# Optimization experiments

Hardware: AMD Instinct MI355X
Metric: run time of the kernel (lower is better)

## Reference

```python
import jax, jax.numpy as jnp
import numpy as np

B, T, N, D, L, TE, F, H = 32, 1024, 256, 512, 512, 512, 2048, 8

PARAM_SHAPES = {
    "sa_norm_g": (D,), "sa_norm_b": (D,),
    "sa_q_w": (D, D), "sa_q_b": (D,), "sa_k_w": (D, D), "sa_k_b": (D,), "sa_v_w": (D, D), "sa_v_b": (D,),
    "sa_emb_w": (TE, 2 * D), "sa_emb_b": (2 * D,), "sa_pnorm_g": (D,), "sa_pnorm_b": (D,),
    "sa_out_w": (D, D), "sa_out_b": (D,),
    "ca_norm_g": (D,), "ca_norm_b": (D,), "ca_tnorm_g": (L,), "ca_tnorm_b": (L,),
    "ca_q_w": (D, D), "ca_q_b": (D,), "ca_k_w": (L, D), "ca_k_b": (D,), "ca_v_w": (L, D), "ca_v_b": (D,),
    "ca_emb_w": (TE, 2 * D), "ca_emb_b": (2 * D,), "ca_pnorm_g": (D,), "ca_pnorm_b": (D,),
    "ca_out_w": (D, D), "ca_out_b": (D,),
    "ffn_w1": (D, F), "ffn_b1": (F,), "ffn_w2": (F, D), "ffn_b2": (D,),
    "ffn_emb_w": (TE, 2 * D), "ffn_emb_b": (2 * D,), "ffn_pnorm_g": (D,), "ffn_pnorm_b": (D,),
    "ffn_out_w": (D, D), "ffn_out_b": (D,),
}


def setup_inputs() -> dict:
    key = jax.random.key(0)
    inp = {}
    inp["x"] = jax.random.normal(jax.random.fold_in(key, 100), (B, T, D), jnp.float32)
    inp["xf"] = jax.random.normal(jax.random.fold_in(key, 101), (B, N, L), jnp.float32)
    inp["emb"] = jax.random.normal(jax.random.fold_in(key, 102), (B, TE), jnp.float32)
    inp["src_mask"] = (jax.random.uniform(jax.random.fold_in(key, 103), (B, T, 1)) < 0.9).astype(jnp.float32)
    for i, (name, shp) in enumerate(PARAM_SHAPES.items()):
        k = jax.random.fold_in(key, i)
        if name.endswith("norm_g") or name.endswith("pnorm_g") or name.endswith("tnorm_g"):
            inp[name] = jnp.ones(shp, jnp.float32)
        else:
            inp[name] = 0.02 * jax.random.normal(k, shp, jnp.float32)
    return inp


def _ln(v, g, b):
    mu = jnp.mean(v, -1, keepdims=True)
    var = jnp.mean(jnp.square(v - mu), -1, keepdims=True)
    return (v - mu) * jax.lax.rsqrt(var + 1e-5) * g + b


def _styl(h, emb, ew, eb, ng, nb, ow, ob):
    # StylizationBlock: AdaLN scale-shift then SiLU + linear (dropout = identity at eval)
    e = (jax.nn.silu(emb) @ ew + eb)[:, None, :]          # [B, 1, 2D]
    scale, shift = jnp.split(e, 2, axis=-1)
    hn = _ln(h, ng, nb) * (1.0 + scale) + shift
    return jax.nn.silu(hn) @ ow + ob


def _lin_attn(q, k, v):
    # Performer-style: contract over sequence first -> [B,H,d,dl], then apply queries
    att = jnp.einsum('bnhd,bnhl->bhdl', k, v)
    return jnp.einsum('bthd,bhdl->bthl', q, att)


def _forward(x, xf, emb, src_mask, sa_norm_g, sa_norm_b, sa_q_w, sa_q_b, sa_k_w, sa_k_b, sa_v_w, sa_v_b, sa_emb_w, sa_emb_b, sa_pnorm_g, sa_pnorm_b, sa_out_w, sa_out_b, ca_norm_g, ca_norm_b, ca_tnorm_g, ca_tnorm_b, ca_q_w, ca_q_b, ca_k_w, ca_k_b, ca_v_w, ca_v_b, ca_emb_w, ca_emb_b, ca_pnorm_g, ca_pnorm_b, ca_out_w, ca_out_b, ffn_w1, ffn_b1, ffn_w2, ffn_b2, ffn_emb_w, ffn_emb_b, ffn_pnorm_g, ffn_pnorm_b, ffn_out_w, ffn_out_b):
    B_, T_, D_ = x.shape
    d = D_ // H
    # ---- linear temporal self-attention ----
    xn = _ln(x, sa_norm_g, sa_norm_b)
    q = jax.nn.softmax((xn @ sa_q_w + sa_q_b).reshape(B_, T_, H, d), axis=-1)   # softmax over feature dim
    k = jax.nn.softmax((xn @ sa_k_w + sa_k_b + (1.0 - src_mask) * -1000000.0).reshape(B_, T_, H, d), axis=1)  # softmax over seq
    v = ((xn @ sa_v_w + sa_v_b) * src_mask).reshape(B_, T_, H, d)
    y = _lin_attn(q, k, v).reshape(B_, T_, D_)
    x = x + _styl(y, emb, sa_emb_w, sa_emb_b, sa_pnorm_g, sa_pnorm_b, sa_out_w, sa_out_b)
    # ---- linear temporal cross-attention ----
    xn = _ln(x, ca_norm_g, ca_norm_b)
    tn = _ln(xf, ca_tnorm_g, ca_tnorm_b)
    N_ = xf.shape[1]
    q = jax.nn.softmax((xn @ ca_q_w + ca_q_b).reshape(B_, T_, H, d), axis=-1)
    k = jax.nn.softmax((tn @ ca_k_w + ca_k_b).reshape(B_, N_, H, d), axis=1)
    v = (tn @ ca_v_w + ca_v_b).reshape(B_, N_, H, d)
    y = _lin_attn(q, k, v).reshape(B_, T_, D_)
    x = x + _styl(y, emb, ca_emb_w, ca_emb_b, ca_pnorm_g, ca_pnorm_b, ca_out_w, ca_out_b)
    # ---- FFN ----
    y = jax.nn.gelu(x @ ffn_w1 + ffn_b1, approximate=False) @ ffn_w2 + ffn_b2
    x = x + _styl(y, emb, ffn_emb_w, ffn_emb_b, ffn_pnorm_g, ffn_pnorm_b, ffn_out_w, ffn_out_b)
    return x


def reference(x, xf, emb, src_mask, sa_norm_g, sa_norm_b, sa_q_w, sa_q_b, sa_k_w, sa_k_b, sa_v_w, sa_v_b, sa_emb_w, sa_emb_b, sa_pnorm_g, sa_pnorm_b, sa_out_w, sa_out_b, ca_norm_g, ca_norm_b, ca_tnorm_g, ca_tnorm_b, ca_q_w, ca_q_b, ca_k_w, ca_k_b, ca_v_w, ca_v_b, ca_emb_w, ca_emb_b, ca_pnorm_g, ca_pnorm_b, ca_out_w, ca_out_b, ffn_w1, ffn_b1, ffn_w2, ffn_b2, ffn_emb_w, ffn_emb_b, ffn_pnorm_g, ffn_pnorm_b, ffn_out_w, ffn_out_b):
    return _forward(x, xf, emb, src_mask, sa_norm_g, sa_norm_b, sa_q_w, sa_q_b, sa_k_w, sa_k_b, sa_v_w, sa_v_b, sa_emb_w, sa_emb_b, sa_pnorm_g, sa_pnorm_b, sa_out_w, sa_out_b, ca_norm_g, ca_norm_b, ca_tnorm_g, ca_tnorm_b, ca_q_w, ca_q_b, ca_k_w, ca_k_b, ca_v_w, ca_v_b, ca_emb_w, ca_emb_b, ca_pnorm_g, ca_pnorm_b, ca_out_w, ca_out_b, ffn_w1, ffn_b1, ffn_w2, ffn_b2, ffn_emb_w, ffn_emb_b, ffn_pnorm_g, ffn_pnorm_b, ffn_out_w, ffn_out_b)
```

## Files before the change

kernel.cpp:

```cpp
#include <hip/hip_runtime.h>
#include <hip/hip_bf16.h>
#include <math.h>

typedef __hip_bfloat16 bf16;
typedef __hip_bfloat162 bf16x2;
using s8 = __attribute__((ext_vector_type(8))) short;
using f4 = __attribute__((ext_vector_type(4))) float;

#define DEV __device__ __forceinline__
DEV float bf2f(bf16 h){ return __bfloat162float(h); }
DEV bf16  f2bf(float f){ return __float2bfloat16(f); }
DEV float silu_f(float x){ return x / (1.0f + __expf(-x)); }
DEV float gelu_f(float x){ return 0.5f * x * (1.0f + erff(x * 0.70710678118654752f)); }

__global__ __launch_bounds__(256) void transpose_w(const float* __restrict__ in,
                                                   bf16* __restrict__ out, int K, int N){
  __shared__ float t[32][33];
  int n0 = blockIdx.x * 32, k0 = blockIdx.y * 32;
  int tx = threadIdx.x, ty = threadIdx.y;
  for (int i = ty; i < 32; i += 8) t[i][tx] = in[(size_t)(k0 + i) * N + n0 + tx];
  __syncthreads();
  for (int i = ty; i < 32; i += 8) out[(size_t)(n0 + i) * K + k0 + tx] = f2bf(t[tx][i]);
}

__global__ __launch_bounds__(256) void ln_kernel(const float* __restrict__ in, bf16* __restrict__ out,
                                                 const float* __restrict__ g, const float* __restrict__ b){
  int row = blockIdx.x, tid = threadIdx.x;
  const float* r = in + (size_t)row * 512;
  float2 v = *(const float2*)&r[tid * 2];
  float s = v.x + v.y, s2 = v.x * v.x + v.y * v.y;
  #pragma unroll
  for (int o = 1; o < 64; o <<= 1){ s += __shfl_xor(s, o); s2 += __shfl_xor(s2, o); }
  __shared__ float rs[4], rs2[4];
  int w = tid >> 6;
  if ((tid & 63) == 0){ rs[w] = s; rs2[w] = s2; }
  __syncthreads();
  s  = rs[0] + rs[1] + rs[2] + rs[3];
  s2 = rs2[0] + rs2[1] + rs2[2] + rs2[3];
  float mu = s * (1.0f / 512.0f);
  float var = fmaxf(s2 * (1.0f / 512.0f) - mu * mu, 0.0f);
  float rstd = rsqrtf(var + 1e-5f);
  int c = tid * 2;
  bf16x2 o;
  o.x = f2bf((v.x - mu) * rstd * g[c]     + b[c]);
  o.y = f2bf((v.y - mu) * rstd * g[c + 1] + b[c + 1]);
  *(bf16x2*)&out[(size_t)row * 512 + c] = o;
}

__global__ __launch_bounds__(256) void styl_ln_kernel(const bf16* __restrict__ in, const float* __restrict__ e,
                                                      const float* __restrict__ g, const float* __restrict__ b,
                                                      bf16* __restrict__ out, int T){
  int row = blockIdx.x, tid = threadIdx.x;
  int bidx = row / T;
  const bf16* r = in + (size_t)row * 512;
  bf16x2 hv = *(const bf16x2*)&r[tid * 2];
  float x0 = bf2f(hv.x), x1 = bf2f(hv.y);
  float s = x0 + x1, s2 = x0 * x0 + x1 * x1;
  #pragma unroll
  for (int o = 1; o < 64; o <<= 1){ s += __shfl_xor(s, o); s2 += __shfl_xor(s2, o); }
  __shared__ float rs[4], rs2[4];
  int w = tid >> 6;
  if ((tid & 63) == 0){ rs[w] = s; rs2[w] = s2; }
  __syncthreads();
  s  = rs[0] + rs[1] + rs[2] + rs[3];
  s2 = rs2[0] + rs2[1] + rs2[2] + rs2[3];
  float mu = s * (1.0f / 512.0f);
  float var = fmaxf(s2 * (1.0f / 512.0f) - mu * mu, 0.0f);
  float rstd = rsqrtf(var + 1e-5f);
  int c = tid * 2;
  const float* eb = e + (size_t)bidx * 1024;
  float h0 = (x0 - mu) * rstd * g[c]     + b[c];
  float h1 = (x1 - mu) * rstd * g[c + 1] + b[c + 1];
  h0 = h0 * (1.0f + eb[c])     + eb[512 + c];
  h1 = h1 * (1.0f + eb[c + 1]) + eb[512 + c + 1];
  bf16x2 o; o.x = f2bf(silu_f(h0)); o.y = f2bf(silu_f(h1));
  *(bf16x2*)&out[(size_t)row * 512 + c] = o;
}

__global__ __launch_bounds__(256) void kv_outer(const bf16* __restrict__ k, const bf16* __restrict__ v,
                                                const float* __restrict__ mask,
                                                float* __restrict__ att_part, float* __restrict__ den_part,
                                                int T, int ld, int Tc){
  int bh = blockIdx.x;
  int b = bh >> 3, h = bh & 7;
  int chunk = blockIdx.y;
  int t_begin = chunk * Tc;
  __shared__ float kexp[64][64];
  __shared__ bf16 vb[64][64];
  int tid = threadIdx.x;
  int lg = tid & 15, tg = tid >> 4;
  int d0 = tg * 4, l0 = lg * 4;
  const float* mrow = mask ? (mask + (size_t)b * T) : nullptr;
  float acc[4][4] = {};
  float sden[4] = {0.0f, 0.0f, 0.0f, 0.0f};
  for (int tcb = t_begin; tcb < t_begin + Tc; tcb += 64){
    __syncthreads();
    #pragma unroll
    for (int i = 0; i < 2; ++i){
      int rr = (tid >> 3) + i * 32;
      int cc = (tid & 7) * 8;
      size_t goff = ((size_t)(b * T + tcb + rr)) * ld + h * 64 + cc;
      s8 kv8 = *(const s8*)&k[goff];
      *(s8*)&vb[rr][cc] = *(const s8*)&v[goff];
      float mk = mrow ? mrow[tcb + rr] : 1.0f;
      float4 e0, e1;
      e0.x = mk * __expf(bf2f(((const bf16*)&kv8)[0]));
      e0.y = mk * __expf(bf2f(((const bf16*)&kv8)[1]));
      e0.z = mk * __expf(bf2f(((const bf16*)&kv8)[2]));
      e0.w = mk * __expf(bf2f(((const bf16*)&kv8)[3]));
      e1.x = mk * __expf(bf2f(((const bf16*)&kv8)[4]));
      e1.y = mk * __expf(bf2f(((const bf16*)&kv8)[5]));
      e1.z = mk * __expf(bf2f(((const bf16*)&kv8)[6]));
      e1.w = mk * __expf(bf2f(((const bf16*)&kv8)[7]));
      *(float4*)&kexp[rr][cc]     = e0;
      *(float4*)&kexp[rr][cc + 4] = e1;
    }
    __syncthreads();
    for (int tt = 0; tt < 64; ++tt){
      float4 kf = *(const float4*)&kexp[tt][d0];
      float kk[4] = {kf.x, kf.y, kf.z, kf.w};
      float vv[4];
      #pragma unroll
      for (int j = 0; j < 4; ++j) vv[j] = bf2f(vb[tt][l0 + j]);
      #pragma unroll
      for (int a = 0; a < 4; ++a){
        sden[a] += kk[a];
        #pragma unroll
        for (int c2 = 0; c2 < 4; ++c2) acc[a][c2] += kk[a] * vv[c2];
      }
    }
  }
  size_t base = ((size_t)(chunk * 256 + bh)) * 4096;
  #pragma unroll
  for (int a = 0; a < 4; ++a)
    #pragma unroll
    for (int c2 = 0; c2 < 4; ++c2) att_part[base + (size_t)(d0 + a) * 64 + l0 + c2] = acc[a][c2];
  if (lg == 0){
    size_t dbase = ((size_t)(chunk * 256 + bh)) * 64;
    #pragma unroll
    for (int a = 0; a < 4; ++a) den_part[dbase + d0 + a] = sden[a];
  }
}

__global__ __launch_bounds__(256) void kv_reduce(const float* __restrict__ att_part,
                                                 const float* __restrict__ den_part,
                                                 float* __restrict__ att, int nchunk){
  int bh = blockIdx.x, tid = threadIdx.x;
  __shared__ float dinv[64];
  if (tid < 64){
    float d = 0.0f;
    for (int c = 0; c < nchunk; ++c) d += den_part[((size_t)(c * 256 + bh)) * 64 + tid];
    dinv[tid] = 1.0f / d;
  }
  __syncthreads();
  #pragma unroll
  for (int i = 0; i < 16; ++i){
    int e = i * 256 + tid;
    float s = 0.0f;
    for (int c = 0; c < nchunk; ++c) s += att_part[((size_t)(c * 256 + bh)) * 4096 + e];
    att[(size_t)bh * 4096 + e] = s * dinv[e >> 6];
  }
}

__global__ __launch_bounds__(256) void q_att(const bf16* __restrict__ q, const float* __restrict__ att,
                                             bf16* __restrict__ y, int T, int ldq){
  int ntc = T >> 6;
  int idx = blockIdx.x;
  int tcb = idx % ntc; int h = (idx / ntc) & 7; int b = idx / (ntc * 8);
  __shared__ float ab[64][64];
  __shared__ bf16 qb[64][64];
  int tid = threadIdx.x;
  #pragma unroll
  for (int i = 0; i < 4; ++i){
    int e = i * 1024 + tid * 4;
    *(float4*)&ab[e >> 6][e & 63] = *(const float4*)&att[((size_t)(b * 8 + h)) * 4096 + e];
  }
  #pragma unroll
  for (int i = 0; i < 2; ++i){
    int rr = (tid >> 3) + i * 32;
    int cc = (tid & 7) * 8;
    s8 v = *(const s8*)&q[((size_t)(b * T + tcb * 64 + rr)) * ldq + h * 64 + cc];
    float f[8];
    #pragma unroll
    for (int j = 0; j < 8; ++j) f[j] = bf2f(((const bf16*)&v)[j]);
    float m = f[0];
    #pragma unroll
    for (int j = 1; j < 8; ++j) m = fmaxf(m, f[j]);
    m = fmaxf(m, __shfl_xor(m, 1));
    m = fmaxf(m, __shfl_xor(m, 2));
    m = fmaxf(m, __shfl_xor(m, 4));
    float s = 0.0f;
    #pragma unroll
    for (int j = 0; j < 8; ++j){ f[j] = __expf(f[j] - m); s += f[j]; }
    s += __shfl_xor(s, 1);
    s += __shfl_xor(s, 2);
    s += __shfl_xor(s, 4);
    float inv = 1.0f / s;
    s8 o;
    #pragma unroll
    for (int j = 0; j < 8; ++j) ((bf16*)&o)[j] = f2bf(f[j] * inv);
    *(s8*)&qb[rr][cc ^ ((rr & 7) << 3)] = o;
  }
  __syncthreads();
  int lg = tid & 15, tg = tid >> 4;
  int t0 = tg * 4, l0 = lg * 4;
  float acc[4][4] = {};
  for (int dd = 0; dd < 64; ++dd){
    float qv[4], av[4];
    #pragma unroll
    for (int j = 0; j < 4; ++j){
      int row = t0 + j;
      qv[j] = bf2f(qb[row][dd ^ ((row & 7) << 3)]);
      av[j] = ab[dd][l0 + j];
    }
    #pragma unroll
    for (int a = 0; a < 4; ++a)
      #pragma unroll
      for (int c2 = 0; c2 < 4; ++c2) acc[a][c2] += qv[a] * av[c2];
  }
  #pragma unroll
  for (int a = 0; a < 4; ++a)
    #pragma unroll
    for (int c2 = 0; c2 < 4; ++c2)
      y[((size_t)(b * T + tcb * 64 + t0 + a)) * 512 + h * 64 + l0 + c2] = f2bf(acc[a][c2]);
}

__global__ __launch_bounds__(256) void emb_gemm(const float* __restrict__ emb,
    const float* __restrict__ w0, const float* __restrict__ b0,
    const float* __restrict__ w1, const float* __restrict__ b1,
    const float* __restrict__ w2, const float* __restrict__ b2,
    float* __restrict__ e_all){
  int col = blockIdx.x * 256 + threadIdx.x;
  int b = blockIdx.y, which = blockIdx.z;
  const float* W  = (which == 0) ? w0 : (which == 1 ? w1 : w2);
  const float* bb = (which == 0) ? b0 : (which == 1 ? b1 : b2);
  __shared__ float s[512];
  for (int i = threadIdx.x; i < 512; i += 256){ float v = emb[b * 512 + i]; s[i] = silu_f(v); }
  __syncthreads();
  float acc = bb[col];
  for (int kk = 0; kk < 512; ++kk) acc += s[kk] * W[(size_t)kk * 1024 + col];
  e_all[((size_t)which * 32 + b) * 1024 + col] = acc;
}

template<int EPI>
__global__ __launch_bounds__(256, 2) void gemm_bt(
    const bf16* __restrict__ A, const bf16* __restrict__ BT,
    const float* __restrict__ bias, void* __restrict__ out,
    const float* __restrict__ extra, void* __restrict__ out2, int M, int N, int K){
  __shared__ __align__(16) bf16 As[2][128 * 32];
  __shared__ __align__(16) bf16 Bs[2][128 * 32];
  int tid = threadIdx.x;
  int w = tid >> 6, lane = tid & 63;
  int wr = w >> 1, wc = w & 1;
  int nwg = gridDim.x * gridDim.y;
  int lin = blockIdx.y * gridDim.x + blockIdx.x;
  int xcd = lin & 7, sidx = lin >> 3;
  int q8 = nwg >> 3, r8 = nwg & 7;
  int wg = (xcd < r8 ? xcd * (q8 + 1) : r8 * (q8 + 1) + (xcd - r8) * q8) + sidx;
  int bn = wg % gridDim.x, bm = wg / gridDim.x;

  const bf16* Ab = A  + (size_t)bm * 128 * K;
  const bf16* Bb = BT + (size_t)bn * 128 * K;

  int srow = tid >> 2;
  int scol = (tid & 3) * 8;

  auto stage = [&](int buf, int k0){
    #pragma unroll
    for (int i = 0; i < 2; ++i){
      const bf16* ga = Ab + (size_t)(srow + i * 64) * K + k0 + scol;
      const bf16* gb = Bb + (size_t)(srow + i * 64) * K + k0 + scol;
      bf16* la = &As[buf][i * 2048 + w * 512];
      bf16* lb = &Bs[buf][i * 2048 + w * 512];
      __builtin_amdgcn_global_load_lds((const __attribute__((address_space(1))) void*)ga,
                                       (__attribute__((address_space(3))) void*)la, 16, 0, 0);
      __builtin_amdgcn_global_load_lds((const __attribute__((address_space(1))) void*)gb,
                                       (__attribute__((address_space(3))) void*)lb, 16, 0, 0);
    }
  };

  f4 acc[4][4];
  #pragma unroll
  for (int m = 0; m < 4; ++m)
    #pragma unroll
    for (int n = 0; n < 4; ++n)
      #pragma unroll
      for (int j = 0; j < 4; ++j) acc[m][n][j] = 0.0f;

  int nt = K >> 5;
  int arow = lane & 15;
  int koff = (lane >> 4) * 8;

  stage(0, 0);
  __syncthreads();
  int cur = 0;
  for (int t = 0; t < nt; ++t){
    if (t + 1 < nt) stage(cur ^ 1, (t + 1) * 32);
    s8 af[4], bfv[4];
    #pragma unroll
    for (int m = 0; m < 4; ++m)
      af[m] = *(const s8*)&As[cur][(wr * 64 + m * 16 + arow) * 32 + koff];
    #pragma unroll
    for (int n = 0; n < 4; ++n)
      bfv[n] = *(const s8*)&Bs[cur][(wc * 64 + n * 16 + arow) * 32 + koff];
    #pragma unroll
    for (int m = 0; m < 4; ++m)
      #pragma unroll
      for (int n = 0; n < 4; ++n)
        acc[m][n] = __builtin_amdgcn_mfma_f32_16x16x32_bf16(af[m], bfv[n], acc[m][n], 0, 0, 0);
    __syncthreads();
    cur ^= 1;
  }

  int r0 = bm * 128 + wr * 64 + (lane >> 4) * 4;
  int c0 = bn * 128 + wc * 64 + (lane & 15);
  #pragma unroll
  for (int m = 0; m < 4; ++m){
    #pragma unroll
    for (int n = 0; n < 4; ++n){
      int col = c0 + n * 16;
      float bv = bias[col];
      #pragma unroll
      for (int j = 0; j < 4; ++j){
        int row = r0 + m * 16 + j;
        float v = acc[m][n][j] + bv;
        size_t oi = (size_t)row * N + col;
        if (EPI == 0){
          ((bf16*)out)[oi] = f2bf(v);
        } else if (EPI == 2){
          ((bf16*)out)[oi] = f2bf(gelu_f(v));
        } else if (EPI == 3){
          ((float*)out)[oi] += v;
        } else if (EPI == 4){
          ((float*)out)[oi] = extra[oi] + v;
        } else if (EPI == 5){
          float nv = ((float*)out)[oi] + v;
          ((float*)out)[oi] = nv;
          ((bf16*)out2)[oi] = f2bf(nv);
        } else {
          float sc = (col >= 1024) ? extra[row] : 1.0f;
          ((bf16*)out)[oi] = f2bf(v * sc);
        }
      }
    }
  }
}

extern "C" void kernel_launch(void* const* d_in, const int* in_sizes, int n_in,
                              void* d_out, int out_size, void* d_ws, size_t ws_size,
                              hipStream_t stream){
  const float* x    = (const float*)d_in[0];
  const float* xf   = (const float*)d_in[1];
  const float* emb  = (const float*)d_in[2];
  const float* mask = (const float*)d_in[3];
  const float* P[40];
  for (int j = 0; j < 40; ++j) P[j] = (const float*)d_in[4 + j];
  enum { SA_NG, SA_NB, SA_QW, SA_QB, SA_KW, SA_KB, SA_VW, SA_VB, SA_EW, SA_EB, SA_PG, SA_PB, SA_OW, SA_OB,
         CA_NG, CA_NB, CA_TG, CA_TB, CA_QW, CA_QB, CA_KW, CA_KB, CA_VW, CA_VB, CA_EW, CA_EB, CA_PG, CA_PB, CA_OW, CA_OB,
         F_W1, F_B1, F_W2, F_B2, F_EW, F_EB, F_PG, F_PB, F_OW, F_OB };

  char* wp = (char*)d_ws;
  auto alloc = [&](size_t bytes){ void* p = (void*)wp; wp += (bytes + 255) & ~(size_t)255; return p; };

  const size_t SQ = (size_t)512 * 512 * 2;
  bf16* WT_saqkv = (bf16*)alloc(3 * SQ);
  bf16* WT_saout = (bf16*)alloc(SQ);
  bf16* WT_caq   = (bf16*)alloc(SQ);
  bf16* WT_cakv  = (bf16*)alloc(2 * SQ);
  bf16* WT_caout = (bf16*)alloc(SQ);
  bf16* WT_f1    = (bf16*)alloc((size_t)2048 * 512 * 2);
  bf16* WT_f2    = (bf16*)alloc((size_t)512 * 2048 * 2);
  bf16* WT_fout  = (bf16*)alloc(SQ);
  float* cat_sab = (float*)alloc(1536 * 4);
  float* cat_cab = (float*)alloc(1024 * 4);
  float* e_all   = (float*)alloc((size_t)3 * 32 * 1024 * 4);

  const size_t BTD2 = (size_t)32768 * 512 * 2;
  bf16* bxn  = (bf16*)alloc(BTD2);
  bf16* bqkv = (bf16*)alloc(3 * BTD2);
  bf16* by   = (bf16*)alloc(BTD2);
  bf16* bs   = (bf16*)alloc(BTD2);
  bf16* btn  = (bf16*)alloc((size_t)8192 * 512 * 2);
  float* att_part = (float*)alloc((size_t)4 * 256 * 4096 * 4);
  float* den_part = (float*)alloc((size_t)4 * 256 * 64 * 4);
  float* batt = (float*)alloc((size_t)256 * 4096 * 4);
  bf16* bh1 = bxn;
  bf16* bq_ca  = bqkv;
  bf16* bkv_ca = bqkv + BTD2 / 2;

  dim3 tb(32, 8);
  transpose_w<<<dim3(16, 16), tb, 0, stream>>>(P[SA_QW], WT_saqkv,               512, 512);
  transpose_w<<<dim3(16, 16), tb, 0, stream>>>(P[SA_KW], WT_saqkv + 512 * 512,   512, 512);
  transpose_w<<<dim3(16, 16), tb, 0, stream>>>(P[SA_VW], WT_saqkv + 1024 * 512,  512, 512);
  transpose_w<<<dim3(16, 16), tb, 0, stream>>>(P[SA_OW], WT_saout, 512, 512);
  transpose_w<<<dim3(16, 16), tb, 0, stream>>>(P[CA_QW], WT_caq, 512, 512);
  transpose_w<<<dim3(16, 16), tb, 0, stream>>>(P[CA_KW], WT_cakv,             512, 512);
  transpose_w<<<dim3(16, 16), tb, 0, stream>>>(P[CA_VW], WT_cakv + 512 * 512, 512, 512);
  transpose_w<<<dim3(16, 16), tb, 0, stream>>>(P[CA_OW], WT_caout, 512, 512);
  transpose_w<<<dim3(64, 16), tb, 0, stream>>>(P[F_W1], WT_f1, 512, 2048);
  transpose_w<<<dim3(16, 64), tb, 0, stream>>>(P[F_W2], WT_f2, 2048, 512);
  transpose_w<<<dim3(16, 16), tb, 0, stream>>>(P[F_OW], WT_fout, 512, 512);

  hipMemcpyAsync(cat_sab,        P[SA_QB], 512 * 4, hipMemcpyDeviceToDevice, stream);
  hipMemcpyAsync(cat_sab + 512,  P[SA_KB], 512 * 4, hipMemcpyDeviceToDevice, stream);
  hipMemcpyAsync(cat_sab + 1024, P[SA_VB], 512 * 4, hipMemcpyDeviceToDevice, stream);
  hipMemcpyAsync(cat_cab,        P[CA_KB], 512 * 4, hipMemcpyDeviceToDevice, stream);
  hipMemcpyAsync(cat_cab + 512,  P[CA_VB], 512 * 4, hipMemcpyDeviceToDevice, stream);

  emb_gemm<<<dim3(4, 32, 3), 256, 0, stream>>>(emb, P[SA_EW], P[SA_EB], P[CA_EW], P[CA_EB],
                                               P[F_EW], P[F_EB], e_all);

  dim3 g512(4, 256);

  ln_kernel<<<32768, 256, 0, stream>>>(x, bxn, P[SA_NG], P[SA_NB]);
  gemm_bt<6><<<dim3(12, 256), 256, 0, stream>>>(bxn, WT_saqkv, cat_sab, bqkv, mask, nullptr, 32768, 1536, 512);
  kv_outer<<<dim3(256, 4), 256, 0, stream>>>(bqkv + 512, bqkv + 1024, mask, att_part, den_part, 1024, 1536, 256);
  kv_reduce<<<256, 256, 0, stream>>>(att_part, den_part, batt, 4);
  q_att<<<4096, 256, 0, stream>>>(bqkv, batt, by, 1024, 1536);
  styl_ln_kernel<<<32768, 256, 0, stream>>>(by, e_all, P[SA_PG], P[SA_PB], bs, 1024);
  gemm_bt<4><<<g512, 256, 0, stream>>>(bs, WT_saout, P[SA_OB], d_out, x, nullptr, 32768, 512, 512);

  ln_kernel<<<32768, 256, 0, stream>>>((const float*)d_out, bxn, P[CA_NG], P[CA_NB]);
  ln_kernel<<<8192, 256, 0, stream>>>(xf, btn, P[CA_TG], P[CA_TB]);
  gemm_bt<0><<<g512, 256, 0, stream>>>(bxn, WT_caq, P[CA_QB], bq_ca, nullptr, nullptr, 32768, 512, 512);
  gemm_bt<0><<<dim3(8, 64), 256, 0, stream>>>(btn, WT_cakv, cat_cab, bkv_ca, nullptr, nullptr, 8192, 1024, 512);
  kv_outer<<<dim3(256, 2), 256, 0, stream>>>(bkv_ca, bkv_ca + 512, nullptr, att_part, den_part, 256, 1024, 128);
  kv_reduce<<<256, 256, 0, stream>>>(att_part, den_part, batt, 2);
  q_att<<<4096, 256, 0, stream>>>(bq_ca, batt, by, 1024, 512);
  styl_ln_kernel<<<32768, 256, 0, stream>>>(by, e_all + 32 * 1024, P[CA_PG], P[CA_PB], bs, 1024);
  gemm_bt<5><<<g512, 256, 0, stream>>>(bs, WT_caout, P[CA_OB], d_out, nullptr, bs, 32768, 512, 512);

  gemm_bt<2><<<dim3(16, 256), 256, 0, stream>>>(bs, WT_f1, P[F_B1], bh1, nullptr, nullptr, 32768, 2048, 512);
  gemm_bt<0><<<dim3(4, 256), 256, 0, stream>>>(bh1, WT_f2, P[F_B2], by, nullptr, nullptr, 32768, 512, 2048);
  styl_ln_kernel<<<32768, 256, 0, stream>>>(by, e_all + 2 * 32 * 1024, P[F_PG], P[F_PB], bs, 1024);
  gemm_bt<3><<<g512, 256, 0, stream>>>(bs, WT_fout, P[F_OB], d_out, nullptr, nullptr, 32768, 512, 512);
}
```

Measured before the change: 907.1 us.

## Replace 128x128 GEMM with 256x256 tile, swizzled LDS, phased MFMA kernel

Rewrites the bf16 GEMM to use 256x256 output tiles with 512 threads, 64-wide K stages, an XOR-swizzled LDS layout and a phased fragment-load/MFMA schedule with wave priority hints. Larger tiles raise arithmetic intensity and cut global/LDS traffic per flop, and the swizzle avoids LDS bank conflicts. All GEMM launches get new grid sizes. The 128KB of shared memory and many accumulators limit occupancy, and small grids (e.g. the cross-attention KV projection) may underfill the CUs.

```diff
diff --git a/kernel.cpp b/kernel.cpp
--- a/kernel.cpp
+++ b/kernel.cpp
@@ -242,16 +242,36 @@
   e_all[((size_t)which * 32 + b) * 1024 + col] = acc;
 }
 
+#define GFENCE asm volatile("" ::: "memory")
+#define DRAIN_BAR asm volatile("s_waitcnt vmcnt(0)\n\ts_barrier" ::: "memory")
+
+#define PHASE_MFMA(QM, QN, AARR, BARR)                                                  \
+  __builtin_amdgcn_s_setprio(1);                                                        \
+  _Pragma("unroll")                                                                     \
+  for (int fm_ = 0; fm_ < 4; ++fm_){                                                    \
+    _Pragma("unroll")                                                                   \
+    for (int fn_ = 0; fn_ < 2; ++fn_){                                                  \
+      acc[(QM)*4+fm_][(QN)*2+fn_] = __builtin_amdgcn_mfma_f32_16x16x32_bf16(            \
+          AARR[fm_][0], BARR[fn_][0], acc[(QM)*4+fm_][(QN)*2+fn_], 0, 0, 0);            \
+      acc[(QM)*4+fm_][(QN)*2+fn_] = __builtin_amdgcn_mfma_f32_16x16x32_bf16(            \
+          AARR[fm_][1], BARR[fn_][1], acc[(QM)*4+fm_][(QN)*2+fn_], 0, 0, 0);            \
+    }                                                                                   \
+  }                                                                                     \
+  __builtin_amdgcn_s_setprio(0);
+
 template<int EPI>
-__global__ __launch_bounds__(256, 2) void gemm_bt(
+__global__ __launch_bounds__(512, 2) void gemm256(
     const bf16* __restrict__ A, const bf16* __restrict__ BT,
     const float* __restrict__ bias, void* __restrict__ out,
-    const float* __restrict__ extra, void* __restrict__ out2, int M, int N, int K){
-  __shared__ __align__(16) bf16 As[2][128 * 32];
-  __shared__ __align__(16) bf16 Bs[2][128 * 32];
+    const float* __restrict__ extra, void* __restrict__ out2,
+    int M, int N, int K){
+  __shared__ __align__(16) bf16 As[2][256 * 64];
+  __shared__ __align__(16) bf16 Bs[2][256 * 64];
+  const int BUFB = 32768;
   int tid = threadIdx.x;
-  int w = tid >> 6, lane = tid & 63;
-  int wr = w >> 1, wc = w & 1;
+  int wv = tid >> 6, l = tid & 63;
+  int wm = wv >> 2, wn = wv & 3;
+
   int nwg = gridDim.x * gridDim.y;
   int lin = blockIdx.y * gridDim.x + blockIdx.x;
   int xcd = lin & 7, sidx = lin >> 3;
@@ -259,71 +279,91 @@
   int wg = (xcd < r8 ? xcd * (q8 + 1) : r8 * (q8 + 1) + (xcd - r8) * q8) + sidx;
   int bn = wg % gridDim.x, bm = wg / gridDim.x;
 
-  const bf16* Ab = A  + (size_t)bm * 128 * K;
-  const bf16* Bb = BT + (size_t)bn * 128 * K;
-
-  int srow = tid >> 2;
-  int scol = (tid & 3) * 8;
+  const bf16* Ab = A  + (size_t)bm * 256 * K;
+  const bf16* Bb = BT + (size_t)bn * 256 * K;
+
+  int srow = tid >> 3;
+  int kgsrc = ((tid & 7) ^ (srow & 7)) * 8;
 
   auto stage = [&](int buf, int k0){
     #pragma unroll
-    for (int i = 0; i < 2; ++i){
-      const bf16* ga = Ab + (size_t)(srow + i * 64) * K + k0 + scol;
-      const bf16* gb = Bb + (size_t)(srow + i * 64) * K + k0 + scol;
-      bf16* la = &As[buf][i * 2048 + w * 512];
-      bf16* lb = &Bs[buf][i * 2048 + w * 512];
-      __builtin_amdgcn_global_load_lds((const __attribute__((address_space(1))) void*)ga,
-                                       (__attribute__((address_space(3))) void*)la, 16, 0, 0);
-      __builtin_amdgcn_global_load_lds((const __attribute__((address_space(1))) void*)gb,
-                                       (__attribute__((address_space(3))) void*)lb, 16, 0, 0);
+    for (int h = 0; h < 2; ++h){
+      #pragma unroll
+      for (int i = 0; i < 2; ++i){
+        const bf16* ga = Ab + (size_t)(h * 128 + i * 64 + srow) * K + k0 + kgsrc;
+        const bf16* gb = Bb + (size_t)(h * 128 + i * 64 + srow) * K + k0 + kgsrc;
+        char* da = (char*)&As[0][0] + buf * BUFB + h * 16384 + i * 8192 + wv * 1024;
+        char* db = (char*)&Bs[0][0] + buf * BUFB + h * 16384 + i * 8192 + wv * 1024;
+        __builtin_amdgcn_global_load_lds((const __attribute__((address_space(1))) void*)ga,
+                                         (__attribute__((address_space(3))) void*)da, 16, 0, 0);
+        __builtin_amdgcn_global_load_lds((const __attribute__((address_space(1))) void*)gb,
+                                         (__attribute__((address_space(3))) void*)db, 16, 0, 0);
+      }
     }
   };
 
-  f4 acc[4][4];
-  #pragma unroll
-  for (int m = 0; m < 4; ++m)
+  int arow = l & 15;
+  int kof0 = (((l >> 4)       ^ (l & 7)) << 4);
+  int kof1 = ((((l >> 4) + 4) ^ (l & 7)) << 4);
+  const char* AbaseL = (const char*)&As[0][0] + (size_t)(wm * 128 + arow) * 128;
+  const char* BbaseL = (const char*)&Bs[0][0] + (size_t)(wn * 64 + arow) * 128;
+
+  s8 aF[4][2], bF0[2][2], bF1[2][2];
+  auto loadA = [&](int buf, int q){
+    const char* p = AbaseL + buf * BUFB + q * 8192;
+    #pragma unroll
+    for (int fm = 0; fm < 4; ++fm){
+      aF[fm][0] = *(const s8*)(p + fm * 2048 + kof0);
+      aF[fm][1] = *(const s8*)(p + fm * 2048 + kof1);
+    }
+  };
+  auto loadB = [&](s8 (&bF)[2][2], int buf, int q){
+    const char* p = BbaseL + buf * BUFB + q * 4096;
+    #pragma unroll
+    for (int fn = 0; fn < 2; ++fn){
+      bF[fn][0] = *(const s8*)(p + fn * 2048 + kof0);
+      bF[fn][1] = *(const s8*)(p + fn * 2048 + kof1);
+    }
+  };
+
+  f4 acc[8][4];
+  #pragma unroll
+  for (int m = 0; m < 8; ++m)
     #pragma unroll
     for (int n = 0; n < 4; ++n)
       #pragma unroll
       for (int j = 0; j < 4; ++j) acc[m][n][j] = 0.0f;
 
-  int nt = K >> 5;
-  int arow = lane & 15;
-  int koff = (lane >> 4) * 8;
-
   stage(0, 0);
-  __syncthreads();
-  int cur = 0;
+  DRAIN_BAR;
+
+  int nt = K >> 6;
   for (int t = 0; t < nt; ++t){
-    if (t + 1 < nt) stage(cur ^ 1, (t + 1) * 32);
-    s8 af[4], bfv[4];
-    #pragma unroll
-    for (int m = 0; m < 4; ++m)
-      af[m] = *(const s8*)&As[cur][(wr * 64 + m * 16 + arow) * 32 + koff];
-    #pragma unroll
-    for (int n = 0; n < 4; ++n)
-      bfv[n] = *(const s8*)&Bs[cur][(wc * 64 + n * 16 + arow) * 32 + koff];
-    #pragma unroll
-    for (int m = 0; m < 4; ++m)
-      #pragma unroll
-      for (int n = 0; n < 4; ++n)
-        acc[m][n] = __builtin_amdgcn_mfma_f32_16x16x32_bf16(af[m], bfv[n], acc[m][n], 0, 0, 0);
-    __syncthreads();
-    cur ^= 1;
-  }
-
-  int r0 = bm * 128 + wr * 64 + (lane >> 4) * 4;
-  int c0 = bn * 128 + wc * 64 + (lane & 15);
-  #pragma unroll
-  for (int m = 0; m < 4; ++m){
-    #pragma unroll
-    for (int n = 0; n < 4; ++n){
-      int col = c0 + n * 16;
+    int c = t & 1;
+    if (t + 1 < nt){ stage(c ^ 1, (t + 1) << 6); GFENCE; }
+    loadA(c, 0);
+    loadB(bF0, c, 0);
+    PHASE_MFMA(0, 0, aF, bF0);
+    loadB(bF1, c, 1);
+    PHASE_MFMA(0, 1, aF, bF1);
+    loadA(c, 1);
+    PHASE_MFMA(1, 1, aF, bF1);
+    PHASE_MFMA(1, 0, aF, bF0);
+    DRAIN_BAR;
+  }
+
+  int r0 = bm * 256 + wm * 128 + (l >> 4) * 4;
+  int c0 = bn * 256 + wn * 64 + (l & 15);
+  #pragma unroll
+  for (int fm = 0; fm < 8; ++fm){
+    #pragma unroll
+    for (int fn = 0; fn < 4; ++fn){
+      int col = c0 + fn * 16;
       float bv = bias[col];
       #pragma unroll
       for (int j = 0; j < 4; ++j){
-        int row = r0 + m * 16 + j;
-        float v = acc[m][n][j] + bv;
+        int row = r0 + fm * 16 + j;
+        float v = acc[fm][fn][j] + bv;
         size_t oi = (size_t)row * N + col;
         if (EPI == 0){
           ((bf16*)out)[oi] = f2bf(v);
@@ -410,28 +450,28 @@
   emb_gemm<<<dim3(4, 32, 3), 256, 0, stream>>>(emb, P[SA_EW], P[SA_EB], P[CA_EW], P[CA_EB],
                                                P[F_EW], P[F_EB], e_all);
 
-  dim3 g512(4, 256);
+  dim3 g512(2, 128);
 
   ln_kernel<<<32768, 256, 0, stream>>>(x, bxn, P[SA_NG], P[SA_NB]);
-  gemm_bt<6><<<dim3(12, 256), 256, 0, stream>>>(bxn, WT_saqkv, cat_sab, bqkv, mask, nullptr, 32768, 1536, 512);
+  gemm256<6><<<dim3(6, 128), 512, 0, stream>>>(bxn, WT_saqkv, cat_sab, bqkv, mask, nullptr, 32768, 1536, 512);
   kv_outer<<<dim3(256, 4), 256, 0, stream>>>(bqkv + 512, bqkv + 1024, mask, att_part, den_part, 1024, 1536, 256);
   kv_reduce<<<256, 256, 0, stream>>>(att_part, den_part, batt, 4);
   q_att<<<4096, 256, 0, stream>>>(bqkv, batt, by, 1024, 1536);
   styl_ln_kernel<<<32768, 256, 0, stream>>>(by, e_all, P[SA_PG], P[SA_PB], bs, 1024);
-  gemm_bt<4><<<g512, 256, 0, stream>>>(bs, WT_saout, P[SA_OB], d_out, x, nullptr, 32768, 512, 512);
+  gemm256<4><<<g512, 512, 0, stream>>>(bs, WT_saout, P[SA_OB], d_out, x, nullptr, 32768, 512, 512);
 
   ln_kernel<<<32768, 256, 0, stream>>>((const float*)d_out, bxn, P[CA_NG], P[CA_NB]);
   ln_kernel<<<8192, 256, 0, stream>>>(xf, btn, P[CA_TG], P[CA_TB]);
-  gemm_bt<0><<<g512, 256, 0, stream>>>(bxn, WT_caq, P[CA_QB], bq_ca, nullptr, nullptr, 32768, 512, 512);
-  gemm_bt<0><<<dim3(8, 64), 256, 0, stream>>>(btn, WT_cakv, cat_cab, bkv_ca, nullptr, nullptr, 8192, 1024, 512);
+  gemm256<0><<<g512, 512, 0, stream>>>(bxn, WT_caq, P[CA_QB], bq_ca, nullptr, nullptr, 32768, 512, 512);
+  gemm256<0><<<dim3(4, 32), 512, 0, stream>>>(btn, WT_cakv, cat_cab, bkv_ca, nullptr, nullptr, 8192, 1024, 512);
   kv_outer<<<dim3(256, 2), 256, 0, stream>>>(bkv_ca, bkv_ca + 512, nullptr, att_part, den_part, 256, 1024, 128);
   kv_reduce<<<256, 256, 0, stream>>>(att_part, den_part, batt, 2);
   q_att<<<4096, 256, 0, stream>>>(bq_ca, batt, by, 1024, 512);
   styl_ln_kernel<<<32768, 256, 0, stream>>>(by, e_all + 32 * 1024, P[CA_PG], P[CA_PB], bs, 1024);
-  gemm_bt<5><<<g512, 256, 0, stream>>>(bs, WT_caout, P[CA_OB], d_out, nullptr, bs, 32768, 512, 512);
-
-  gemm_bt<2><<<dim3(16, 256), 256, 0, stream>>>(bs, WT_f1, P[F_B1], bh1, nullptr, nullptr, 32768, 2048, 512);
-  gemm_bt<0><<<dim3(4, 256), 256, 0, stream>>>(bh1, WT_f2, P[F_B2], by, nullptr, nullptr, 32768, 512, 2048);
+  gemm256<5><<<g512, 512, 0, stream>>>(bs, WT_caout, P[CA_OB], d_out, nullptr, bs, 32768, 512, 512);
+
+  gemm256<2><<<dim3(8, 128), 512, 0, stream>>>(bs, WT_f1, P[F_B1], bh1, nullptr, nullptr, 32768, 2048, 512);
+  gemm256<0><<<g512, 512, 0, stream>>>(bh1, WT_f2, P[F_B2], by, nullptr, nullptr, 32768, 512, 2048);
   styl_ln_kernel<<<32768, 256, 0, stream>>>(by, e_all + 2 * 32 * 1024, P[F_PG], P[F_PB], bs, 1024);
-  gemm_bt<3><<<g512, 256, 0, stream>>>(bs, WT_fout, P[F_OB], d_out, nullptr, nullptr, 32768, 512, 512);
-}
+  gemm256<3><<<g512, 512, 0, stream>>>(bs, WT_fout, P[F_OB], d_out, nullptr, nullptr, 32768, 512, 512);
+}
```

Result: slower. 986.0 us (+8.7%).
